# Kernel optimization log

Measured on AMD Instinct MI355X. Metric: run time of the kernel, lower is better.

## Reference

```python
import jax, jax.numpy as jnp
import numpy as np

N_NODES = 50000
N_EDGES = 800000
F_IN = 32
F_OUT = 32
NB = 4  # basis terms per dimension


def linear_basis(x, n):
    # Piecewise-linear 'hat' basis on [-1, 1] with n equispaced centers.
    # f_k(x) = max(0, 1 - |x - c_k| / dx),  c_k = linspace(-1, 1, n), dx = 2/(n-1)
    centers = jnp.linspace(-1.0, 1.0, n, dtype=x.dtype)
    dx = 2.0 / (n - 1)
    return jnp.maximum(0.0, 1.0 - jnp.abs(x[:, None] - centers) / dx)  # [E, n]


def setup_inputs() -> dict:
    key = jax.random.key(0)
    k0, k1, k2, k3, k4 = jax.random.split(key, 5)
    x_i = jax.random.normal(k0, (N_NODES, F_IN), dtype=jnp.float32)
    x_j = jax.random.normal(k1, (N_NODES, F_IN), dtype=jnp.float32)
    edge_index = jax.random.randint(k2, (2, N_EDGES), 0, N_NODES)  # row0=target, row1=source
    edge_attr = jax.random.uniform(k3, (N_EDGES, 2), dtype=jnp.float32,
                                   minval=-1.0, maxval=1.0)
    # torch init: uniform_(-0.05, 0.05) on [NB, NB, F_IN, F_OUT]
    weight = jax.random.uniform(k4, (NB, NB, F_IN, F_OUT), dtype=jnp.float32,
                                minval=-0.05, maxval=0.05)
    return {"x_i": x_i, "x_j": x_j, "edge_index": edge_index,
            "edge_attr": edge_attr, "weight": weight}


def reference(x_i, x_j, edge_index, edge_attr, weight):
    dst = edge_index[0]  # aggregation target nodes
    src = edge_index[1]  # source nodes (features gathered from x_j)

    bx = linear_basis(edge_attr[:, 0], NB)            # [E, NB]
    by = linear_basis(edge_attr[:, 1], NB)            # [E, NB]
    b = (bx[:, :, None] * by[:, None, :]).reshape(-1, NB * NB)  # [E, NB*NB]

    feat = x_j[src]                                   # [E, F_IN] edge gather
    w = weight.reshape(NB * NB, F_IN, F_OUT)          # [K, F_IN, F_OUT]
    msg = jnp.einsum('ek,ei,kio->eo', b, feat, w)     # [E, F_OUT]

    # weighted scatter-add to target nodes
    out = jax.ops.segment_sum(msg, dst, num_segments=x_i.shape[0])  # [N, F_OUT]
    return out
```

## Files before the change

### kernel.cpp

```cpp
#include <hip/hip_runtime.h>
#include <hip/hip_bf16.h>

typedef short short8 __attribute__((ext_vector_type(8)));
typedef float f32x4 __attribute__((ext_vector_type(4)));
typedef unsigned uint4v __attribute__((ext_vector_type(4)));

#define F 32
#define NB 4
#define BINSH 5
#define BINSZ 32
#define EPB 512
#define SCH 4096
#define MAXBIN 2048
#define CAPB 2048
#define OSCH 2048
#define OMAXNBLK 1024

__device__ __forceinline__ short f2bf(float f) {
    unsigned u = __float_as_uint(f);
    unsigned r = (u + 0x7FFFu + ((u >> 16) & 1u)) >> 16;
    return (short)r;
}

__device__ __forceinline__ unsigned pk2(float a, float b) {
    __hip_bfloat162 h = __float22bfloat162_rn(make_float2(a, b));
    union { __hip_bfloat162 h; unsigned u; } cv; cv.h = h; return cv.u;
}

__global__ __launch_bounds__(256) void zero_kernel(int* __restrict__ p, int n) {
    for (int i = threadIdx.x; i < n; i += 256) p[i] = 0;
}

__global__ __launch_bounds__(256) void w_prep(
    const float* __restrict__ w, short* __restrict__ wbf)
{
    int idx = blockIdx.x * 256 + threadIdx.x;
    int k = idx >> 10, rem = idx & 1023, i = rem >> 5, o = rem & 31;
    int slot = (((k * 4 + (i >> 3)) * 2 + (o >> 4)) * 16 + (o & 15)) * 8 + (i & 7);
    wbf[slot] = f2bf(w[idx]);
}

__global__ __launch_bounds__(256) void h2_kernel(
    const int* __restrict__ ei, const float* __restrict__ attr, int E, int nbin,
    int* __restrict__ bincnt, int* __restrict__ cellcnt)
{
    __shared__ int hb[MAXBIN];
    __shared__ int hc[9];
    int t = threadIdx.x;
    for (int i = t; i < nbin; i += 256) hb[i] = 0;
    if (t < 9) hc[t] = 0;
    __syncthreads();
    int stride = gridDim.x * blockDim.x;
    for (int e = blockIdx.x * blockDim.x + t; e < E; e += stride) {
        int dst = ei[e];
        float2 a = reinterpret_cast<const float2*>(attr)[e];
        float tx = fminf(fmaxf((a.x + 1.0f) * 1.5f, 0.f), 3.f);
        float ty = fminf(fmaxf((a.y + 1.0f) * 1.5f, 0.f), 3.f);
        int kx = min((int)tx, 2), ky = min((int)ty, 2);
        atomicAdd(&hb[dst >> BINSH], 1);
        atomicAdd(&hc[kx * 3 + ky], 1);
    }
    __syncthreads();
    for (int i = t; i < nbin; i += 256)
        if (hb[i]) atomicAdd(&bincnt[i], hb[i]);
    if (t < 9 && hc[t]) atomicAdd(&cellcnt[t], hc[t]);
}

__global__ __launch_bounds__(256) void scan2_kernel(
    const int* __restrict__ bincnt, int* __restrict__ binbase,
    int* __restrict__ bincur, const int* __restrict__ cellcnt,
    int* __restrict__ cellbase, int* __restrict__ cellcur,
    int* __restrict__ blkoff, int nbin)
{
    __shared__ int part[256];
    int t = threadIdx.x;
    int chunk = (nbin + 255) / 256;
    int lo = t * chunk, hi = min(lo + chunk, nbin);
    int s = 0;
    for (int q = lo; q < hi; ++q) s += bincnt[q];
    part[t] = s;
    __syncthreads();
    if (t == 0) {
        int run = 0;
        for (int j = 0; j < 256; ++j) { int v = part[j]; part[j] = run; run += v; }
        binbase[nbin] = run;
    }
    __syncthreads();
    int run = part[t];
    for (int q = lo; q < hi; ++q) {
        binbase[q] = run; bincur[q] = run;
        run += bincnt[q];
    }
    if (t == 0) {
        int off = 0, boff = 0;
        for (int c = 0; c < 9; ++c) {
            cellbase[c] = off; cellcur[c] = off; blkoff[c] = boff;
            off  += cellcnt[c];
            boff += (cellcnt[c] + EPB - 1) / EPB;
        }
        cellbase[9] = off; blkoff[9] = boff;
    }
}

__global__ __launch_bounds__(256) void scat2_kernel(
    const int* __restrict__ ei, const float* __restrict__ attr, int E, int nbin,
    int* __restrict__ bincur, int* __restrict__ cellcur,
    uint4* __restrict__ cellrec, unsigned char* __restrict__ dloc8)
{
    __shared__ int hb[MAXBIN];
    __shared__ int hc[9];
    int t = threadIdx.x, b = blockIdx.x;
    int start = b * SCH, end = min(start + SCH, E);
    for (int i = t; i < nbin; i += 256) hb[i] = 0;
    if (t < 9) hc[t] = 0;
    __syncthreads();
    for (int e = start + t; e < end; e += 256) {
        int dst = ei[e];
        float2 a = reinterpret_cast<const float2*>(attr)[e];
        float tx = fminf(fmaxf((a.x + 1.0f) * 1.5f, 0.f), 3.f);
        float ty = fminf(fmaxf((a.y + 1.0f) * 1.5f, 0.f), 3.f);
        int kx = min((int)tx, 2), ky = min((int)ty, 2);
        atomicAdd(&hb[dst >> BINSH], 1);
        atomicAdd(&hc[kx * 3 + ky], 1);
    }
    __syncthreads();
    for (int k = t; k < nbin; k += 256) {
        int c = hb[k];
        if (c) hb[k] = atomicAdd(&bincur[k], c);
    }
    if (t < 9) hc[t] = atomicAdd(&cellcur[t], hc[t]);
    __syncthreads();
    for (int e = start + t; e < end; e += 256) {
        int dst = ei[e];
        int src = ei[E + e];
        float2 a = reinterpret_cast<const float2*>(attr)[e];
        float tx = fminf(fmaxf((a.x + 1.0f) * 1.5f, 0.f), 3.f);
        float ty = fminf(fmaxf((a.y + 1.0f) * 1.5f, 0.f), 3.f);
        int kx = min((int)tx, 2), ky = min((int)ty, 2);
        int pd = atomicAdd(&hb[dst >> BINSH], 1);
        int pc = atomicAdd(&hc[kx * 3 + ky], 1);
        uint4 rec;
        rec.x = (unsigned)src;
        rec.y = (unsigned)pd;
        rec.z = __float_as_uint(tx);
        rec.w = __float_as_uint(ty);
        cellrec[pc] = rec;
        dloc8[pd] = (unsigned char)(dst & (BINSZ - 1));
    }
}

__global__ __launch_bounds__(256, 4) void bconv_msg(
    const float* __restrict__ x_j, const short* __restrict__ wbf,
    const int* __restrict__ cellbase, const int* __restrict__ blkoff,
    const uint4* __restrict__ cellrec, unsigned* __restrict__ msg)
{
    int b = blockIdx.x;
    if (b >= blkoff[9]) return;
    int c = 0;
    #pragma unroll
    for (int q = 1; q < 9; ++q) c += (b >= blkoff[q]) ? 1 : 0;
    int kx0 = c / 3, ky0 = c - 3 * (c / 3);
    int local  = b - blkoff[c];
    int cstart = cellbase[c], cend = cellbase[c + 1];
    int pstart = cstart + local * EPB;
    int pend   = min(pstart + EPB, cend);
    if (pstart >= pend) return;

    int t = threadIdx.x;
    int wid = t >> 6, lane = t & 63;
    int row16 = lane & 15, hi = lane >> 4;

    short8 w0[4], w1[4];
    #pragma unroll
    for (int kk = 0; kk < 4; ++kk) {
        int ks = (kx0 + (kk >> 1)) * NB + (ky0 + (kk & 1));
        w0[kk] = *reinterpret_cast<const short8*>(
            wbf + (((ks * 4 + hi) * 2 + 0) * 16 + row16) * 8);
        w1[kk] = *reinterpret_cast<const short8*>(
            wbf + (((ks * 4 + hi) * 2 + 1) * 16 + row16) * 8);
    }

    const float4* x4 = reinterpret_cast<const float4*>(x_j);
    int ntile = (pend - pstart + 15) >> 4;

    auto fetch = [&](int ti, uint4& rec, float4& fa, float4& fb, int& pdv) {
        int p = pstart + ti * 16 + row16;
        bool v = p < pend;
        int pp = v ? p : pstart;
        rec = cellrec[pp];
        int src = rec.x;
        fa = x4[src * 8 + 2 * hi];
        fb = x4[src * 8 + 2 * hi + 1];
        pdv = v ? (int)rec.y : -1;
    };

    int it = wid;
    uint4 rec; float4 fa, fb; int pdv;
    if (it < ntile) fetch(it, rec, fa, fb, pdv);

    for (; it < ntile; it += 4) {
        uint4 recN; float4 faN, fbN; int pdvN = -1;
        bool hn = (it + 4) < ntile;
        if (hn) fetch(it + 4, recN, faN, fbN, pdvN);

        float tx = __uint_as_float(rec.z), ty = __uint_as_float(rec.w);
        float fx = tx - (float)kx0, fy = ty - (float)ky0;
        float bx0 = 1.f - fx, by0 = 1.f - fy;
        float bc[4] = { bx0 * by0, bx0 * fy, fx * by0, fx * fy };
        float fl[8] = { fa.x, fa.y, fa.z, fa.w, fb.x, fb.y, fb.z, fb.w };

        f32x4 a0 = {0,0,0,0}, a1 = {0,0,0,0};
        #pragma unroll
        for (int kk = 0; kk < 4; ++kk) {
            float s = bc[kk];
            uint4v u;
            u[0] = pk2(fl[0] * s, fl[1] * s);
            u[1] = pk2(fl[2] * s, fl[3] * s);
            u[2] = pk2(fl[4] * s, fl[5] * s);
            u[3] = pk2(fl[6] * s, fl[7] * s);
            short8 av = __builtin_bit_cast(short8, u);
            a0 = __builtin_amdgcn_mfma_f32_16x16x32_bf16(av, w0[kk], a0, 0, 0, 0);
            a1 = __builtin_amdgcn_mfma_f32_16x16x32_bf16(av, w1[kk], a1, 0, 0, 0);
        }
        #pragma unroll
        for (int r = 0; r < 4; ++r) {
            int pd = __shfl(pdv, 4 * hi + r, 64);
            if (pd >= 0)
                msg[(size_t)pd * 16 + row16] = pk2(a0[r], a1[r]);
        }
        rec = recN; fa = faN; fb = fbN; pdv = pdvN;
    }
}

__global__ __launch_bounds__(256, 8) void bconv_reduce(
    const unsigned* __restrict__ msg, const unsigned char* __restrict__ dloc8,
    const int* __restrict__ binbase, float* __restrict__ out, int N)
{
    __shared__ unsigned short perm[CAPB];
    __shared__ int cnt[32], cbase[33], cur[32];

    int t = threadIdx.x, bin = blockIdx.x;
    int g = t >> 3, j = t & 7;
    int s0 = binbase[bin], s1 = binbase[bin + 1];
    const uint2* m2 = reinterpret_cast<const uint2*>(msg);

    float aAlo = 0.f, aAhi = 0.f, aBlo = 0.f, aBhi = 0.f;

    for (int chunk = s0; chunk < s1; chunk += CAPB) {
        int clen = min(CAPB, s1 - chunk);
        if (t < 32) cnt[t] = 0;
        __syncthreads();
        for (int i = t; i < clen; i += 256)
            atomicAdd(&cnt[dloc8[chunk + i]], 1);
        __syncthreads();
        if (t == 0) {
            int run = 0;
            #pragma unroll
            for (int c2 = 0; c2 < 32; ++c2) { cbase[c2] = run; run += cnt[c2]; }
            cbase[32] = run;
        }
        __syncthreads();
        if (t < 32) cur[t] = cbase[t];
        __syncthreads();
        for (int i = t; i < clen; i += 256) {
            int d = dloc8[chunk + i];
            int r = atomicAdd(&cur[d], 1);
            perm[r] = (unsigned short)i;
        }
        __syncthreads();

        int lo = cbase[g], hi2 = cbase[g + 1];
        int k = lo;
        for (; k + 3 < hi2; k += 4) {
            int i0 = perm[k], i1 = perm[k + 1], i2 = perm[k + 2], i3 = perm[k + 3];
            uint2 v0 = m2[(size_t)(chunk + i0) * 8 + j];
            uint2 v1 = m2[(size_t)(chunk + i1) * 8 + j];
            uint2 v2 = m2[(size_t)(chunk + i2) * 8 + j];
            uint2 v3 = m2[(size_t)(chunk + i3) * 8 + j];
            aAlo += __uint_as_float(v0.x << 16); aAhi += __uint_as_float(v0.x & 0xFFFF0000u);
            aBlo += __uint_as_float(v0.y << 16); aBhi += __uint_as_float(v0.y & 0xFFFF0000u);
            aAlo += __uint_as_float(v1.x << 16); aAhi += __uint_as_float(v1.x & 0xFFFF0000u);
            aBlo += __uint_as_float(v1.y << 16); aBhi += __uint_as_float(v1.y & 0xFFFF0000u);
            aAlo += __uint_as_float(v2.x << 16); aAhi += __uint_as_float(v2.x & 0xFFFF0000u);
            aBlo += __uint_as_float(v2.y << 16); aBhi += __uint_as_float(v2.y & 0xFFFF0000u);
            aAlo += __uint_as_float(v3.x << 16); aAhi += __uint_as_float(v3.x & 0xFFFF0000u);
            aBlo += __uint_as_float(v3.y << 16); aBhi += __uint_as_float(v3.y & 0xFFFF0000u);
        }
        for (; k < hi2; ++k) {
            int i0 = perm[k];
            uint2 v0 = m2[(size_t)(chunk + i0) * 8 + j];
            aAlo += __uint_as_float(v0.x << 16); aAhi += __uint_as_float(v0.x & 0xFFFF0000u);
            aBlo += __uint_as_float(v0.y << 16); aBhi += __uint_as_float(v0.y & 0xFFFF0000u);
        }
        __syncthreads();
    }

    int node = bin * BINSZ + g;
    if (node < N) {
        float2 lo2; lo2.x = aAlo; lo2.y = aBlo;
        float2 hi2v; hi2v.x = aAhi; hi2v.y = aBhi;
        *reinterpret_cast<float2*>(&out[(size_t)node * F + 2 * j])      = lo2;
        *reinterpret_cast<float2*>(&out[(size_t)node * F + 16 + 2 * j]) = hi2v;
    }
}

__global__ __launch_bounds__(256) void hist_kernel(
    const float* __restrict__ attr, int E, int* __restrict__ counts)
{
    __shared__ int hh[9];
    int b = blockIdx.x, t = threadIdx.x;
    if (t < 9) hh[t] = 0;
    __syncthreads();
    int start = b * OSCH, end = min(start + OSCH, E);
    for (int e = start + t; e < end; e += 256) {
        float2 a = reinterpret_cast<const float2*>(attr)[e];
        float tx = fminf(fmaxf((a.x + 1.0f) * 1.5f, 0.f), 3.f);
        float ty = fminf(fmaxf((a.y + 1.0f) * 1.5f, 0.f), 3.f);
        atomicAdd(&hh[min((int)tx, 2) * 3 + min((int)ty, 2)], 1);
    }
    __syncthreads();
    if (t < 9) counts[b * 9 + t] = hh[t];
}

__global__ __launch_bounds__(512) void scan_kernel(
    int* __restrict__ ws, int* __restrict__ counts, int nblk)
{
    __shared__ int s[OMAXNBLK * 9];
    __shared__ int tot[9];
    __shared__ int coff[9];
    int n = nblk * 9;
    for (int i = threadIdx.x; i < n; i += 512) s[i] = counts[i];
    __syncthreads();
    if (threadIdx.x < 9) {
        int c = threadIdx.x, run = 0;
        for (int b = 0; b < nblk; ++b) {
            int v = s[b * 9 + c];
            s[b * 9 + c] = run;
            run += v;
        }
        tot[c] = run;
    }
    __syncthreads();
    if (threadIdx.x == 0) {
        int off = 0, boff = 0;
        for (int c = 0; c < 9; ++c) {
            ws[c] = off;  coff[c] = off;
            ws[16 + c] = boff;
            off  += tot[c];
            boff += (tot[c] + EPB - 1) / EPB;
        }
        ws[9] = off;
        ws[16 + 9] = boff;
    }
    __syncthreads();
    for (int i = threadIdx.x; i < n; i += 512)
        counts[i] = s[i] + coff[i % 9];
}

__global__ __launch_bounds__(256) void scatter_kernel(
    const float* __restrict__ attr, int E,
    const int* __restrict__ bases, int* __restrict__ sorted)
{
    __shared__ int cur9[9];
    int b = blockIdx.x, t = threadIdx.x;
    if (t < 9) cur9[t] = bases[b * 9 + t];
    __syncthreads();
    int start = b * OSCH, end = min(start + OSCH, E);
    for (int e = start + t; e < end; e += 256) {
        float2 a = reinterpret_cast<const float2*>(attr)[e];
        float tx = fminf(fmaxf((a.x + 1.0f) * 1.5f, 0.f), 3.f);
        float ty = fminf(fmaxf((a.y + 1.0f) * 1.5f, 0.f), 3.f);
        int c = min((int)tx, 2) * 3 + min((int)ty, 2);
        int pos = atomicAdd(&cur9[c], 1);
        sorted[pos] = e;
    }
}

__global__ __launch_bounds__(256) void bconv_mfma(
    const float* __restrict__ x_j, const int* __restrict__ ei,
    const float* __restrict__ attr, const float* __restrict__ weight,
    const int* __restrict__ ws, const int* __restrict__ sorted,
    float* __restrict__ out, int E)
{
    int b = blockIdx.x;
    const int* blkoff = ws + 16;
    if (b >= blkoff[9]) return;
    int c = 0;
    #pragma unroll
    for (int q = 1; q < 9; ++q) c += (b >= blkoff[q]) ? 1 : 0;
    int kx0 = c / 3, ky0 = c - 3 * (c / 3);
    int local  = b - blkoff[c];
    int cstart = ws[c], cend = ws[c + 1];
    int pstart = cstart + local * EPB;
    int pend   = min(pstart + EPB, cend);

    int t = threadIdx.x;
    int wid = t >> 6, lane = t & 63;
    int row16 = lane & 15, hi = lane >> 4;

    short8 wb[4][2];
    #pragma unroll
    for (int kk = 0; kk < 4; ++kk) {
        int ks = (kx0 + (kk >> 1)) * NB + (ky0 + (kk & 1));
        const float* wp = weight + (size_t)ks * F * F;
        #pragma unroll
        for (int n = 0; n < 2; ++n) {
            short8 v;
            #pragma unroll
            for (int j = 0; j < 8; ++j)
                v[j] = f2bf(wp[(8 * hi + j) * F + row16 + 16 * n]);
            wb[kk][n] = v;
        }
    }

    int wstart = pstart + wid * (EPB / 4);
    int wend   = min(wstart + (EPB / 4), pend);
    if (wstart >= wend) return;

    int ntiles = (wend - wstart + 15) >> 4;
    for (int tt = 0; tt < ntiles; ++tt) {
        int p = wstart + tt * 16 + row16;
        bool v = p < wend;
        int pp = v ? p : wstart;
        int e  = sorted[pp];
        int dst = ei[e];
        int srcn = ei[E + e];
        float2 a = reinterpret_cast<const float2*>(attr)[e];
        const float4* xr = reinterpret_cast<const float4*>(x_j + (size_t)srcn * F);
        float4 fa = xr[2 * hi];
        float4 fb = xr[2 * hi + 1];

        float fx = (a.x + 1.0f) * 1.5f - (float)kx0;
        float fy = (a.y + 1.0f) * 1.5f - (float)ky0;
        float vs = v ? 1.f : 0.f;
        float bx0 = (1.f - fx) * vs, bx1 = fx * vs;
        float bc[4] = { bx0 * (1.f - fy), bx0 * fy, bx1 * (1.f - fy), bx1 * fy };

        f32x4 a0 = {0,0,0,0}, a1 = {0,0,0,0};
        #pragma unroll
        for (int kk = 0; kk < 4; ++kk) {
            float s = bc[kk];
            uint4v u;
            u[0] = pk2(fa.x * s, fa.y * s);
            u[1] = pk2(fa.z * s, fa.w * s);
            u[2] = pk2(fb.x * s, fb.y * s);
            u[3] = pk2(fb.z * s, fb.w * s);
            short8 av = __builtin_bit_cast(short8, u);
            a0 = __builtin_amdgcn_mfma_f32_16x16x32_bf16(av, wb[kk][0], a0, 0, 0, 0);
            a1 = __builtin_amdgcn_mfma_f32_16x16x32_bf16(av, wb[kk][1], a1, 0, 0, 0);
        }
        #pragma unroll
        for (int r = 0; r < 4; ++r) {
            int d = __shfl(v ? dst : -1, 4 * hi + r, 64);
            if (d >= 0) {
                atomicAdd(&out[(size_t)d * F + row16],      a0[r]);
                atomicAdd(&out[(size_t)d * F + 16 + row16], a1[r]);
            }
        }
    }
}

__global__ __launch_bounds__(256) void bconv_fallback(
    const float* __restrict__ x_j, const int* __restrict__ ei,
    const float* __restrict__ attr, const float* __restrict__ weight,
    float* __restrict__ out, int E)
{
    __shared__ float wl[16 * F * F];
    __shared__ float featl[8][F];
    for (int idx = threadIdx.x; idx < 4096; idx += 256)
        reinterpret_cast<float4*>(wl)[idx] = reinterpret_cast<const float4*>(weight)[idx];
    __syncthreads();

    int lane = threadIdx.x & 31, eslot = threadIdx.x >> 5;
    for (int p = blockIdx.x * 8 + eslot; p < E; p += gridDim.x * 8) {
        int dst = ei[p], srcn = ei[E + p];
        float ax = attr[2 * p], ay = attr[2 * p + 1];
        featl[eslot][lane] = x_j[(size_t)srcn * F + lane];
        float tx = (ax + 1.0f) * 1.5f, ty = (ay + 1.0f) * 1.5f;
        int kx0 = min(max((int)tx, 0), 2), ky0 = min(max((int)ty, 0), 2);
        float fx = tx - kx0, fy = ty - ky0;
        float bcv[4] = { (1.0f - fx) * (1.0f - fy), (1.0f - fx) * fy,
                         fx * (1.0f - fy), fx * fy };
        float msg = 0.f;
        const float4* f4 = reinterpret_cast<const float4*>(&featl[eslot][0]);
        #pragma unroll
        for (int kk = 0; kk < 4; ++kk) {
            int k = (kx0 + (kk >> 1)) * NB + (ky0 + (kk & 1));
            const float* wk = wl + k * F * F;
            float a2 = 0.f;
            #pragma unroll
            for (int j = 0; j < 8; ++j) {
                float4 f = f4[j];
                a2 = fmaf(f.x, wk[(4 * j + 0) * F + lane], a2);
                a2 = fmaf(f.y, wk[(4 * j + 1) * F + lane], a2);
                a2 = fmaf(f.z, wk[(4 * j + 2) * F + lane], a2);
                a2 = fmaf(f.w, wk[(4 * j + 3) * F + lane], a2);
            }
            msg = fmaf(bcv[kk], a2, msg);
        }
        atomicAdd(&out[(size_t)dst * F + lane], msg);
    }
}

extern "C" void kernel_launch(void* const* d_in, const int* in_sizes, int n_in,
                              void* d_out, int out_size, void* d_ws, size_t ws_size,
                              hipStream_t stream) {
    const float* x_j    = (const float*)d_in[1];
    const int*   ei     = (const int*)d_in[2];
    const float* attr   = (const float*)d_in[3];
    const float* weight = (const float*)d_in[4];
    float* out = (float*)d_out;
    int E = in_sizes[2] / 2;
    int N = in_sizes[0] / F;

    int nbin = (N + BINSZ - 1) >> BINSH;

    int o_bincnt   = 0;
    int o_cellcnt  = o_bincnt + nbin;
    int o_binbase  = o_cellcnt + 9;
    int o_bincur   = o_binbase + nbin + 1;
    int o_cellbase = o_bincur + nbin;
    int o_cellcur  = o_cellbase + 10;
    int o_blkoff   = o_cellcur + 9;
    int o_wbf      = (o_blkoff + 10 + 3) & ~3;
    int o_dloc     = o_wbf + 8192;
    int o_cellrec  = (o_dloc + (E + 3) / 4 + 3) & ~3;
    size_t o_msg   = (size_t)((o_cellrec + 4 * (size_t)E + 3) & ~3);
    size_t need_new = (o_msg + 16 * (size_t)E) * sizeof(int);

    int nblk_sort = (E + OSCH - 1) / OSCH;
    int sorted_off = 32 + ((nblk_sort * 9 + 15) & ~15);
    size_t need_old = (size_t)(sorted_off + E) * sizeof(int);

    if (nbin <= MAXBIN && N <= 65536 && E < (1 << 24) && ws_size >= need_new) {
        int* ws = (int*)d_ws;
        short* wbf = (short*)(ws + o_wbf);
        unsigned char* dloc8 = (unsigned char*)(ws + o_dloc);
        uint4* cellrec = (uint4*)(ws + o_cellrec);
        unsigned* msg = (unsigned*)(ws + o_msg);

        zero_kernel<<<1, 256, 0, stream>>>(ws, nbin + 9);
        w_prep<<<64, 256, 0, stream>>>(weight, wbf);
        h2_kernel<<<256, 256, 0, stream>>>(ei, attr, E, nbin,
                                           ws + o_bincnt, ws + o_cellcnt);
        scan2_kernel<<<1, 256, 0, stream>>>(ws + o_bincnt, ws + o_binbase,
                                            ws + o_bincur, ws + o_cellcnt,
                                            ws + o_cellbase, ws + o_cellcur,
                                            ws + o_blkoff, nbin);
        scat2_kernel<<<(E + SCH - 1) / SCH, 256, 0, stream>>>(
            ei, attr, E, nbin, ws + o_bincur, ws + o_cellcur, cellrec, dloc8);
        int nblkA = (E + EPB - 1) / EPB + 9;
        bconv_msg<<<nblkA, 256, 0, stream>>>(x_j, wbf, ws + o_cellbase,
                                             ws + o_blkoff, cellrec, msg);
        bconv_reduce<<<nbin, 256, 0, stream>>>(msg, dloc8, ws + o_binbase, out, N);
    } else if (nblk_sort <= OMAXNBLK && ws_size >= need_old) {
        hipMemsetAsync(d_out, 0, (size_t)out_size * sizeof(float), stream);
        int* ws      = (int*)d_ws;
        int* counts  = ws + 32;
        int* sorted  = ws + sorted_off;
        hist_kernel<<<nblk_sort, 256, 0, stream>>>(attr, E, counts);
        scan_kernel<<<1, 512, 0, stream>>>(ws, counts, nblk_sort);
        scatter_kernel<<<nblk_sort, 256, 0, stream>>>(attr, E, counts, sorted);
        int nblk_main = (E + EPB - 1) / EPB + 9;
        bconv_mfma<<<nblk_main, 256, 0, stream>>>(x_j, ei, attr, weight, ws, sorted, out, E);
    } else {
        hipMemsetAsync(d_out, 0, (size_t)out_size * sizeof(float), stream);
        bconv_fallback<<<2048, 256, 0, stream>>>(x_j, ei, attr, weight, out, E);
    }
}
```

Before: 99.11 us.

## Pack edge records into 8 bytes and deepen message-kernel prefetch

Edge records shrink from 16 to 8 bytes. The source index and position share bit fields with quantized basis coordinates: 16 bits for tx and 12 bits for ty. The message kernel prefetches two tiles ahead instead of one, and message writes use nontemporal stores. This cuts record write and read traffic and hides gather latency, but quantizing the coordinates adds small interpolation error and limits E to below 2^20 on the fast path.

```diff
diff --git a/kernel.cpp b/kernel.cpp
--- a/kernel.cpp
+++ b/kernel.cpp
@@ -105,7 +105,7 @@
 __global__ __launch_bounds__(256) void scat2_kernel(
     const int* __restrict__ ei, const float* __restrict__ attr, int E, int nbin,
     int* __restrict__ bincur, int* __restrict__ cellcur,
-    uint4* __restrict__ cellrec, unsigned char* __restrict__ dloc8)
+    uint2* __restrict__ cellrec, unsigned char* __restrict__ dloc8)
 {
     __shared__ int hb[MAXBIN];
     __shared__ int hc[9];
@@ -139,11 +139,11 @@
         int kx = min((int)tx, 2), ky = min((int)ty, 2);
         int pd = atomicAdd(&hb[dst >> BINSH], 1);
         int pc = atomicAdd(&hc[kx * 3 + ky], 1);
-        uint4 rec;
-        rec.x = (unsigned)src;
-        rec.y = (unsigned)pd;
-        rec.z = __float_as_uint(tx);
-        rec.w = __float_as_uint(ty);
+        unsigned txq = (unsigned)(tx * 21845.0f + 0.5f);
+        unsigned tyq = (unsigned)(ty * 1365.0f + 0.5f);
+        uint2 rec;
+        rec.x = (unsigned)src | (txq << 16);
+        rec.y = (unsigned)pd | (tyq << 20);
         cellrec[pc] = rec;
         dloc8[pd] = (unsigned char)(dst & (BINSZ - 1));
     }
@@ -152,7 +152,7 @@
 __global__ __launch_bounds__(256, 4) void bconv_msg(
     const float* __restrict__ x_j, const short* __restrict__ wbf,
     const int* __restrict__ cellbase, const int* __restrict__ blkoff,
-    const uint4* __restrict__ cellrec, unsigned* __restrict__ msg)
+    const uint2* __restrict__ cellrec, unsigned* __restrict__ msg)
 {
     int b = blockIdx.x;
     if (b >= blkoff[9]) return;
@@ -183,27 +183,20 @@
     const float4* x4 = reinterpret_cast<const float4*>(x_j);
     int ntile = (pend - pstart + 15) >> 4;
 
-    auto fetch = [&](int ti, uint4& rec, float4& fa, float4& fb, int& pdv) {
+    auto fetch = [&](int ti, uint2& rec, float4& fa, float4& fb, int& pdv) {
         int p = pstart + ti * 16 + row16;
         bool v = p < pend;
         int pp = v ? p : pstart;
         rec = cellrec[pp];
-        int src = rec.x;
+        int src = rec.x & 0xFFFF;
         fa = x4[src * 8 + 2 * hi];
         fb = x4[src * 8 + 2 * hi + 1];
-        pdv = v ? (int)rec.y : -1;
+        pdv = v ? (int)(rec.y & 0xFFFFF) : -1;
     };
 
-    int it = wid;
-    uint4 rec; float4 fa, fb; int pdv;
-    if (it < ntile) fetch(it, rec, fa, fb, pdv);
-
-    for (; it < ntile; it += 4) {
-        uint4 recN; float4 faN, fbN; int pdvN = -1;
-        bool hn = (it + 4) < ntile;
-        if (hn) fetch(it + 4, recN, faN, fbN, pdvN);
-
-        float tx = __uint_as_float(rec.z), ty = __uint_as_float(rec.w);
+    auto compute_store = [&](uint2 rec, float4 fa, float4 fb, int pdv) {
+        float tx = (float)(rec.x >> 16) * (1.f / 21845.f);
+        float ty = (float)(rec.y >> 20) * (1.f / 1365.f);
         float fx = tx - (float)kx0, fy = ty - (float)ky0;
         float bx0 = 1.f - fx, by0 = 1.f - fy;
         float bc[4] = { bx0 * by0, bx0 * fy, fx * by0, fx * fy };
@@ -226,9 +219,24 @@
         for (int r = 0; r < 4; ++r) {
             int pd = __shfl(pdv, 4 * hi + r, 64);
             if (pd >= 0)
-                msg[(size_t)pd * 16 + row16] = pk2(a0[r], a1[r]);
-        }
-        rec = recN; fa = faN; fb = fbN; pdv = pdvN;
+                __builtin_nontemporal_store(pk2(a0[r], a1[r]),
+                                            &msg[(size_t)pd * 16 + row16]);
+        }
+    };
+
+    int it = wid;
+    uint2 rA = {0,0}, rB = {0,0};
+    float4 aA = {0,0,0,0}, bA = aA, aB = aA, bB = aA;
+    int pA = -1, pB = -1;
+    if (it < ntile)     fetch(it,     rA, aA, bA, pA);
+    if (it + 4 < ntile) fetch(it + 4, rB, aB, bB, pB);
+
+    for (; it < ntile; it += 4) {
+        uint2 rC = {0,0}; float4 aC = {0,0,0,0}, bC = aC; int pC = -1;
+        if (it + 8 < ntile) fetch(it + 8, rC, aC, bC, pC);
+        compute_store(rA, aA, bA, pA);
+        rA = rB; aA = aB; bA = bB; pA = pB;
+        rB = rC; aB = aC; bB = bC; pB = pC;
     }
 }
 
@@ -524,19 +532,19 @@
     int o_blkoff   = o_cellcur + 9;
     int o_wbf      = (o_blkoff + 10 + 3) & ~3;
     int o_dloc     = o_wbf + 8192;
-    int o_cellrec  = (o_dloc + (E + 3) / 4 + 3) & ~3;
-    size_t o_msg   = (size_t)((o_cellrec + 4 * (size_t)E + 3) & ~3);
+    int o_cellrec  = (o_dloc + (E + 3) / 4 + 1) & ~1;
+    size_t o_msg   = (size_t)((o_cellrec + 2 * (size_t)E + 3) & ~3);
     size_t need_new = (o_msg + 16 * (size_t)E) * sizeof(int);
 
     int nblk_sort = (E + OSCH - 1) / OSCH;
     int sorted_off = 32 + ((nblk_sort * 9 + 15) & ~15);
     size_t need_old = (size_t)(sorted_off + E) * sizeof(int);
 
-    if (nbin <= MAXBIN && N <= 65536 && E < (1 << 24) && ws_size >= need_new) {
+    if (nbin <= MAXBIN && N <= 65536 && E < (1 << 20) && ws_size >= need_new) {
         int* ws = (int*)d_ws;
         short* wbf = (short*)(ws + o_wbf);
         unsigned char* dloc8 = (unsigned char*)(ws + o_dloc);
-        uint4* cellrec = (uint4*)(ws + o_cellrec);
+        uint2* cellrec = (uint2*)(ws + o_cellrec);
         unsigned* msg = (unsigned*)(ws + o_msg);
 
         zero_kernel<<<1, 256, 0, stream>>>(ws, nbin + 9);
```

Result: slower. 118.2 us (+19.2%).
